# Performance work log

Hardware: AMD Instinct MI355X
Metric: run time of the kernel (lower is better)

Reference implementation:

```python
import jax, jax.numpy as jnp
import numpy as np

SIGMA = 0.05  # module init kwarg


def setup_inputs() -> dict:
    key = jax.random.key(0)
    k1, k2 = jax.random.split(key)
    B, N, D = 2, 196, 256
    NUM_SAMPLES = 500
    x = jax.random.normal(k1, (B, N, D), dtype=jnp.float32)
    # noise is generated inside the torch forward; here we pass it explicitly
    # so the reference is deterministic. shape = (B*N, num_samples, D)
    noise = jax.random.normal(k2, (B * N, NUM_SAMPLES, D), dtype=jnp.float32)
    return {"x": x, "noise": noise, "k": 32}


def reference(x, noise, k):
    # Training path of PerturbedTopK (the perturbed estimator).
    B, N, D = x.shape
    x2 = x.reshape(-1, D)                      # (b, d)
    b, n, d = noise.shape
    # perturbed_x: (b, num_samples, d)
    perturbed = x2[:, None, :] + noise * SIGMA
    _, idx = jax.lax.top_k(perturbed, k)       # (b, n, k)
    idx = jnp.sort(idx, axis=-1)               # sorted indices (distinct per row)
    # mean over samples of one_hot(idx, d) == scatter-count / n.
    # Avoids materializing the (b, n, k, d) one-hot tensor; identical math.
    b_idx = jnp.arange(b)[:, None, None]       # (b,1,1)
    k_idx = jnp.arange(k)[None, None, :]       # (1,1,k)
    counts = jnp.zeros((b, k, d), dtype=x.dtype).at[b_idx, k_idx, idx].add(1.0)
    indicators = counts / n                    # (b, k, d)
    return indicators.reshape(B, N, k, D)
```

## Files before the change

### kernel.cpp

```cpp
#include <hip/hip_runtime.h>

#define NROWS 392
#define NSAMP 500
#define DDIM  256
#define KSEL  32
#define SIGMA 0.05f
#define PAIRS (KSEL * DDIM / 2)

__device__ __forceinline__ int mbcnt64(unsigned long long m) {
    int lo = __builtin_amdgcn_mbcnt_lo((unsigned)m, 0u);
    return __builtin_amdgcn_mbcnt_hi((unsigned)(m >> 32), lo);
}

__global__ __launch_bounds__(512) void ptopk_count_kernel(
    const float* __restrict__ x,
    const float* __restrict__ noise,
    unsigned int* __restrict__ partial,
    int split)
{
    __shared__ unsigned int cnt[PAIRS];
    const int tid  = threadIdx.x;
    const int lane = tid & 63;
    const int wid  = tid >> 6;
    const int blk  = blockIdx.x;
    const int row  = blk / split;
    const int chunk = NSAMP / split;
    const int sbeg = (blk % split) * chunk;
    const int send = sbeg + chunk;

    for (int i = tid; i < PAIRS; i += 512) cnt[i] = 0u;

    const float4 xv = *(const float4*)(x + row * DDIM + 4 * lane);
    const float* nrow = noise + (size_t)row * NSAMP * DDIM;
    __syncthreads();

    int s = sbeg + wid;
    float4 nv;
    if (s < send) nv = *(const float4*)(nrow + (size_t)s * DDIM + 4 * lane);

    for (; s < send; s += 8) {
        float4 nvn = nv;
        const int sn = s + 8;
        if (sn < send) nvn = *(const float4*)(nrow + (size_t)sn * DDIM + 4 * lane);

        unsigned int u[4];
        {
            const float v0 = __builtin_fmaf(SIGMA, nv.x, xv.x);
            const float v1 = __builtin_fmaf(SIGMA, nv.y, xv.y);
            const float v2 = __builtin_fmaf(SIGMA, nv.z, xv.z);
            const float v3 = __builtin_fmaf(SIGMA, nv.w, xv.w);
            const float vv[4] = { v0, v1, v2, v3 };
            #pragma unroll
            for (int j = 0; j < 4; ++j) {
                unsigned int b = __float_as_uint(vv[j]);
                u[j] = b ^ ((unsigned)(((int)b) >> 31) | 0x80000000u);
            }
        }

        unsigned int t = 0u;
        for (int bit = 31; bit >= 0; --bit) {
            const unsigned int cand = t | (1u << bit);
            int c = __popcll(__ballot(u[0] >= cand))
                  + __popcll(__ballot(u[1] >= cand))
                  + __popcll(__ballot(u[2] >= cand))
                  + __popcll(__ballot(u[3] >= cand));
            if (c >= KSEL) {
                t = cand;
                if (c == KSEL) break;
            }
        }

        unsigned long long m[4];
        #pragma unroll
        for (int j = 0; j < 4; ++j) m[j] = __ballot(u[j] >= t);
        const int below = mbcnt64(m[0]) + mbcnt64(m[1]) + mbcnt64(m[2]) + mbcnt64(m[3]);

        int own = 0;
        #pragma unroll
        for (int j = 0; j < 4; ++j) {
            if (u[j] >= t) {
                const int r = below + own;
                if (r < KSEL) {
                    atomicAdd(&cnt[r * 128 + 2 * lane + (j >> 1)],
                              (j & 1) ? 0x10000u : 1u);
                }
                ++own;
            }
        }
        nv = nvn;
    }

    __syncthreads();
    unsigned int* dst = partial + (size_t)blk * PAIRS;
    for (int i = tid; i < PAIRS; i += 512) dst[i] = cnt[i];
}

__global__ __launch_bounds__(256) void ptopk_reduce_kernel(
    const unsigned int* __restrict__ partial,
    float2* __restrict__ out, int split, float inv)
{
    const int g   = blockIdx.x * 256 + threadIdx.x;
    const int row = g / PAIRS;
    const int p   = g - row * PAIRS;
    const unsigned int* src = partial + (size_t)(row * split) * PAIRS + p;
    unsigned int lo = 0, hi = 0;
    for (int s = 0; s < split; ++s) {
        const unsigned int w = src[(size_t)s * PAIRS];
        lo += w & 0xFFFFu;
        hi += w >> 16;
    }
    out[g] = make_float2((float)lo * inv, (float)hi * inv);
}

extern "C" void kernel_launch(void* const* d_in, const int* in_sizes, int n_in,
                              void* d_out, int out_size, void* d_ws, size_t ws_size,
                              hipStream_t stream) {
    const float* x     = (const float*)d_in[0];
    const float* noise = (const float*)d_in[1];

    int split = 1;
    if (ws_size >= (size_t)NROWS * 4 * PAIRS * sizeof(unsigned int)) split = 4;
    else if (ws_size >= (size_t)NROWS * 2 * PAIRS * sizeof(unsigned int)) split = 2;

    unsigned int* partial = (unsigned int*)d_ws;

    ptopk_count_kernel<<<NROWS * split, 512, 0, stream>>>(x, noise, partial, split);

    const int npairs = NROWS * PAIRS;
    ptopk_reduce_kernel<<<npairs / 256, 256, 0, stream>>>(
        partial, (float2*)d_out, split, 1.0f / NSAMP);
}
```

Measured before the change: 313.3 us.

## Process two samples per wave iteration with interleaved radix selects; use split of five

Each wave now handles a pair of samples per iteration and interleaves their two bitwise radix-select loops, so the independent ballot chains can overlap and latency is hidden. The sample split per row changes from four to five, so the per-block sample count (100) divides evenly into pairs. The pairing assumes an even chunk size, and the interleaved loop keeps running until both selects finish, so one sample may wait on the slower one. Register pressure rises from holding two noise vectors plus their prefetches.

```diff
diff --git a/kernel.cpp b/kernel.cpp
--- a/kernel.cpp
+++ b/kernel.cpp
@@ -10,6 +10,41 @@
 __device__ __forceinline__ int mbcnt64(unsigned long long m) {
     int lo = __builtin_amdgcn_mbcnt_lo((unsigned)m, 0u);
     return __builtin_amdgcn_mbcnt_hi((unsigned)(m >> 32), lo);
+}
+
+__device__ __forceinline__ void make_u(const float4 nv, const float4 xv, unsigned int u[4]) {
+    const float vv[4] = { __builtin_fmaf(SIGMA, nv.x, xv.x),
+                          __builtin_fmaf(SIGMA, nv.y, xv.y),
+                          __builtin_fmaf(SIGMA, nv.z, xv.z),
+                          __builtin_fmaf(SIGMA, nv.w, xv.w) };
+    #pragma unroll
+    for (int j = 0; j < 4; ++j) {
+        unsigned int b = __float_as_uint(vv[j]);
+        u[j] = b ^ ((unsigned)(((int)b) >> 31) | 0x80000000u);
+    }
+}
+
+__device__ __forceinline__ int count_ge(const unsigned int u[4], unsigned int c) {
+    return __popcll(__ballot(u[0] >= c)) + __popcll(__ballot(u[1] >= c))
+         + __popcll(__ballot(u[2] >= c)) + __popcll(__ballot(u[3] >= c));
+}
+
+__device__ __forceinline__ void scatter(const unsigned int u[4], unsigned int t,
+                                        int lane, unsigned int* cnt) {
+    unsigned long long m[4];
+    #pragma unroll
+    for (int j = 0; j < 4; ++j) m[j] = __ballot(u[j] >= t);
+    const int below = mbcnt64(m[0]) + mbcnt64(m[1]) + mbcnt64(m[2]) + mbcnt64(m[3]);
+    int own = 0;
+    #pragma unroll
+    for (int j = 0; j < 4; ++j) {
+        if (u[j] >= t) {
+            const int r = below + own;
+            if (r < KSEL)
+                atomicAdd(&cnt[r * 128 + 2 * lane + (j >> 1)], (j & 1) ? 0x10000u : 1u);
+            ++own;
+        }
+    }
 }
 
 __global__ __launch_bounds__(512) void ptopk_count_kernel(
@@ -26,68 +61,54 @@
     const int row  = blk / split;
     const int chunk = NSAMP / split;
     const int sbeg = (blk % split) * chunk;
-    const int send = sbeg + chunk;
+    const int npb  = chunk >> 1;
 
     for (int i = tid; i < PAIRS; i += 512) cnt[i] = 0u;
 
     const float4 xv = *(const float4*)(x + row * DDIM + 4 * lane);
-    const float* nrow = noise + (size_t)row * NSAMP * DDIM;
+    const float* nrow = noise + (size_t)row * NSAMP * DDIM + 4 * lane;
     __syncthreads();
 
-    int s = sbeg + wid;
-    float4 nv;
-    if (s < send) nv = *(const float4*)(nrow + (size_t)s * DDIM + 4 * lane);
+    int p = wid;
+    float4 a0, a1;
+    if (p < npb) {
+        a0 = *(const float4*)(nrow + (size_t)(sbeg + 2 * p)     * DDIM);
+        a1 = *(const float4*)(nrow + (size_t)(sbeg + 2 * p + 1) * DDIM);
+    }
 
-    for (; s < send; s += 8) {
-        float4 nvn = nv;
-        const int sn = s + 8;
-        if (sn < send) nvn = *(const float4*)(nrow + (size_t)sn * DDIM + 4 * lane);
-
-        unsigned int u[4];
-        {
-            const float v0 = __builtin_fmaf(SIGMA, nv.x, xv.x);
-            const float v1 = __builtin_fmaf(SIGMA, nv.y, xv.y);
-            const float v2 = __builtin_fmaf(SIGMA, nv.z, xv.z);
-            const float v3 = __builtin_fmaf(SIGMA, nv.w, xv.w);
-            const float vv[4] = { v0, v1, v2, v3 };
-            #pragma unroll
-            for (int j = 0; j < 4; ++j) {
-                unsigned int b = __float_as_uint(vv[j]);
-                u[j] = b ^ ((unsigned)(((int)b) >> 31) | 0x80000000u);
-            }
+    for (; p < npb; p += 8) {
+        float4 b0 = a0, b1 = a1;
+        const int pn = p + 8;
+        if (pn < npb) {
+            b0 = *(const float4*)(nrow + (size_t)(sbeg + 2 * pn)     * DDIM);
+            b1 = *(const float4*)(nrow + (size_t)(sbeg + 2 * pn + 1) * DDIM);
         }
 
-        unsigned int t = 0u;
+        unsigned int u0[4], u1[4];
+        make_u(a0, xv, u0);
+        make_u(a1, xv, u1);
+
+        unsigned int t0 = 0u, t1 = 0u;
+        bool d0 = false, d1 = false;
         for (int bit = 31; bit >= 0; --bit) {
-            const unsigned int cand = t | (1u << bit);
-            int c = __popcll(__ballot(u[0] >= cand))
-                  + __popcll(__ballot(u[1] >= cand))
-                  + __popcll(__ballot(u[2] >= cand))
-                  + __popcll(__ballot(u[3] >= cand));
-            if (c >= KSEL) {
-                t = cand;
-                if (c == KSEL) break;
+            const unsigned int msk = 1u << bit;
+            if (!d0) {
+                const unsigned int c = t0 | msk;
+                const int n = count_ge(u0, c);
+                if (n >= KSEL) { t0 = c; d0 = (n == KSEL); }
             }
+            if (!d1) {
+                const unsigned int c = t1 | msk;
+                const int n = count_ge(u1, c);
+                if (n >= KSEL) { t1 = c; d1 = (n == KSEL); }
+            }
+            if (d0 && d1) break;
         }
 
-        unsigned long long m[4];
-        #pragma unroll
-        for (int j = 0; j < 4; ++j) m[j] = __ballot(u[j] >= t);
-        const int below = mbcnt64(m[0]) + mbcnt64(m[1]) + mbcnt64(m[2]) + mbcnt64(m[3]);
+        scatter(u0, t0, lane, cnt);
+        scatter(u1, t1, lane, cnt);
 
-        int own = 0;
-        #pragma unroll
-        for (int j = 0; j < 4; ++j) {
-            if (u[j] >= t) {
-                const int r = below + own;
-                if (r < KSEL) {
-                    atomicAdd(&cnt[r * 128 + 2 * lane + (j >> 1)],
-                              (j & 1) ? 0x10000u : 1u);
-                }
-                ++own;
-            }
-        }
-        nv = nvn;
+        a0 = b0; a1 = b1;
     }
 
     __syncthreads();
@@ -101,8 +122,8 @@
 {
     const int g   = blockIdx.x * 256 + threadIdx.x;
     const int row = g / PAIRS;
-    const int p   = g - row * PAIRS;
-    const unsigned int* src = partial + (size_t)(row * split) * PAIRS + p;
+    const int pp  = g - row * PAIRS;
+    const unsigned int* src = partial + (size_t)(row * split) * PAIRS + pp;
     unsigned int lo = 0, hi = 0;
     for (int s = 0; s < split; ++s) {
         const unsigned int w = src[(size_t)s * PAIRS];
@@ -118,9 +139,7 @@
     const float* x     = (const float*)d_in[0];
     const float* noise = (const float*)d_in[1];
 
-    int split = 1;
-    if (ws_size >= (size_t)NROWS * 4 * PAIRS * sizeof(unsigned int)) split = 4;
-    else if (ws_size >= (size_t)NROWS * 2 * PAIRS * sizeof(unsigned int)) split = 2;
+    int split = (ws_size >= (size_t)NROWS * 5 * PAIRS * sizeof(unsigned int)) ? 5 : 1;
 
     unsigned int* partial = (unsigned int*)d_ws;
 
```

Result: slower. 320.6 us (+2.3%).
